# Performance work log

Hardware: AMD Instinct MI355X
Metric: run time of the kernel (lower is better)

The kernel has to match this reference:

```python
import jax, jax.numpy as jnp
import numpy as np

HID, HQ, HKV, D, W = 2880, 64, 8, 64, 128  # hidden, q heads, kv heads, head_dim, sliding window
SCALE = D ** -0.5
NEG = -1e30


def _rope(x, cos, sin):
    # x: [B,S,H,D]; cos/sin: [S, D//2]
    c = cos[None, :, None, :].astype(x.dtype)
    s = sin[None, :, None, :].astype(x.dtype)
    x1, x2 = jnp.split(x, 2, axis=-1)
    return jnp.concatenate([x1 * c - x2 * s, x2 * c + x1 * s], axis=-1)


def setup_inputs() -> dict:
    key = jax.random.key(0)
    ks = jax.random.split(key, 12)
    B, S = 1, 4096
    std = 0.02
    x = jax.random.normal(ks[0], (B, S, HID), jnp.float32)
    # realistic rotary table (cos || sin), half-dim each
    inv_freq = 1.0 / (150000.0 ** (np.arange(0, D, 2, dtype=np.float32) / D))
    ang = np.arange(S, dtype=np.float32)[:, None] * inv_freq[None, :]
    freqs_cis = jnp.asarray(np.concatenate([np.cos(ang), np.sin(ang)], axis=-1), jnp.float32)  # [S, D]
    Wq = jax.random.normal(ks[1], (HID, HQ * D), jnp.float32) * std
    bq = jnp.zeros((HQ * D,), jnp.float32)
    Wk = jax.random.normal(ks[2], (HID, HKV * D), jnp.float32) * std
    bk = jnp.zeros((HKV * D,), jnp.float32)
    Wv = jax.random.normal(ks[3], (HID, HKV * D), jnp.float32) * std
    bv = jnp.zeros((HKV * D,), jnp.float32)
    Wo = jax.random.normal(ks[4], (HQ * D, HID), jnp.float32) * std
    bo = jnp.zeros((HID,), jnp.float32)
    sinks = jax.random.normal(ks[5], (HQ,), jnp.float32) * std
    return {"x": x, "freqs_cis": freqs_cis, "Wq": Wq, "bq": bq, "Wk": Wk, "bk": bk,
            "Wv": Wv, "bv": bv, "Wo": Wo, "bo": bo, "sinks": sinks}


def reference(x, freqs_cis, Wq, bq, Wk, bk, Wv, bv, Wo, bo, sinks):
    B, S, _ = x.shape
    G = HQ // HKV
    nb = S // W  # S must be a multiple of W
    cos, sin = jnp.split(freqs_cis, 2, axis=-1)

    q = (x @ Wq + bq).reshape(B, S, HQ, D)
    k = (x @ Wk + bk).reshape(B, S, HKV, D)
    v = (x @ Wv + bv).reshape(B, S, HKV, D)
    q = _rope(q, cos, sin)
    k = _rope(k, cos, sin)

    q = q.transpose(0, 2, 1, 3)  # [B,HQ,S,D]
    k = k.transpose(0, 2, 1, 3)  # [B,HKV,S,D]
    v = v.transpose(0, 2, 1, 3)

    # blocked sliding-window: each query block of size W sees keys [blk*W - W, blk*W + W)
    qb = q.reshape(B, HKV, G, nb, W, D)
    kp = jnp.pad(k, ((0, 0), (0, 0), (W, 0), (0, 0)))  # prepend W zero keys
    vp = jnp.pad(v, ((0, 0), (0, 0), (W, 0), (0, 0)))
    widx = jnp.arange(nb)[:, None] * W + jnp.arange(2 * W)[None, :]  # [nb, 2W]
    kb = kp[:, :, widx]  # [B,HKV,nb,2W,D]
    vb = vp[:, :, widx]

    scores = jnp.einsum('bkgntd,bkncd->bkgntc', qb, kb) * SCALE  # [B,HKV,G,nb,W,2W]

    t = jnp.arange(W)[:, None]
    j = jnp.arange(2 * W)[None, :]
    band = (j >= t + 1) & (j <= t + W)  # 0 <= qpos - kpos <= W-1
    kpos_ok = (jnp.arange(nb)[:, None] * W - W + jnp.arange(2 * W)[None, :]) >= 0  # [nb,2W]
    mask = band[None, :, :] & kpos_ok[:, None, :]  # [nb,W,2W]
    scores = jnp.where(mask[None, None, None], scores, NEG)

    sink = sinks.reshape(HKV, G)[None, :, :, None, None]  # [1,HKV,G,1,1]
    m = jnp.maximum(scores.max(axis=-1), sink)  # [B,HKV,G,nb,W]
    e = jnp.exp(scores - m[..., None])
    denom = e.sum(axis=-1) + jnp.exp(sink - m)
    p = e / denom[..., None]

    o = jnp.einsum('bkgntc,bkncd->bkgntd', p, vb)  # [B,HKV,G,nb,W,D]
    o = o.reshape(B, HQ, S, D).transpose(0, 2, 1, 3).reshape(B, S, HQ * D)
    return o @ Wo + bo
```

## Files before the change

### kernel.cpp

```cpp
#include <hip/hip_runtime.h>
#include <hip/hip_bf16.h>
#include <stdint.h>


typedef __attribute__((ext_vector_type(8))) short bf16x8;
typedef __attribute__((ext_vector_type(4))) float f32x4;
typedef __attribute__((ext_vector_type(8))) unsigned short ushort8;

#define DEVI static __device__ __forceinline__

DEVI unsigned short f2bf(float f) {
  unsigned x = __float_as_uint(f);
  return (unsigned short)((x + 0x7fffu + ((x >> 16) & 1u)) >> 16);
}
DEVI float bf2f(unsigned short u) { return __uint_as_float(((unsigned)u) << 16); }

DEVI void async16(const void* g, void* l) {
  __builtin_amdgcn_global_load_lds(
      (const __attribute__((address_space(1))) void*)g,
      (__attribute__((address_space(3))) void*)l, 16, 0, 0);
}

__global__ void k_cast_bf16(const float* __restrict__ src,
                            unsigned short* __restrict__ dst, long n) {
  long i = ((long)blockIdx.x * blockDim.x + threadIdx.x) * 4;
  const long stride = (long)gridDim.x * blockDim.x * 4;
  for (; i < n; i += stride) {
    float4 v = *(const float4*)(src + i);
    ushort4 o = make_ushort4(f2bf(v.x), f2bf(v.y), f2bf(v.z), f2bf(v.w));
    *(ushort4*)(dst + i) = o;
  }
}

__global__ void k_transpose_cast(const float* __restrict__ src,
                                 unsigned short* __restrict__ dst,
                                 int R, int C) {
  __shared__ float tile[64][65];
  const int t = threadIdx.x;
  const int r0 = blockIdx.y * 64, c0 = blockIdx.x * 64;
#pragma unroll
  for (int i = 0; i < 16; i++) {
    int r = i * 4 + (t >> 6), c = t & 63;
    float v = 0.f;
    if (c0 + c < C) v = src[(long)(r0 + r) * C + c0 + c];
    tile[r][c] = v;
  }
  __syncthreads();
#pragma unroll
  for (int i = 0; i < 16; i++) {
    int nn = i * 4 + (t >> 6), kk = t & 63;
    dst[(long)(c0 + nn) * R + r0 + kk] = f2bf(tile[kk][nn]);
  }
}

__global__ void k_concat_bias(const float* __restrict__ bq,
                              const float* __restrict__ bk,
                              const float* __restrict__ bv,
                              float* __restrict__ dst) {
  int i = blockIdx.x * 256 + threadIdx.x;
  if (i < 5120)
    dst[i] = (i < 4096) ? bq[i] : ((i < 4608) ? bk[i - 4096] : bv[i - 4608]);
}

#define STG(c, half, t)                                                        \
  do {                                                                         \
    const int tt_ = ((t) < NT) ? (t) : NT - 1;                                 \
    const long ko_ = (long)tt_ * 64;                                           \
    if ((half) < 2) {                                                          \
      const unsigned short* s_ = gA + (long)(half) * 128 * Kd + ko_;           \
      unsigned short* d_ = &As_[c][(((half) * 128) + w8) * 64];                \
      async16(s_, d_);                                                         \
      async16(s_ + 64 * (long)Kd, d_ + 64 * 64);                               \
    } else {                                                                   \
      const unsigned short* s_ = gB + (long)((half) - 2) * 128 * Kd + ko_;     \
      unsigned short* d_ = &Bs_[c][((((half) - 2) * 128) + w8) * 64];          \
      async16(s_, d_);                                                         \
      async16(s_ + 64 * (long)Kd, d_ + 64 * 64);                               \
    }                                                                          \
  } while (0)

#define LOADA(c, mh)                                                           \
  do {                                                                         \
    _Pragma("unroll") for (int m4 = 0; m4 < 4; m4++) {                         \
      const unsigned short* r_ =                                               \
          &As_[c][(wr128 + ((mh)*4 + m4) * 16 + ll) * 64];                     \
      aF[m4][0] = *(const bf16x8*)(r_ + sl0 * 8);                              \
      aF[m4][1] = *(const bf16x8*)(r_ + sl1 * 8);                              \
    }                                                                          \
  } while (0)

#define LOADB(c, nh)                                                           \
  do {                                                                         \
    _Pragma("unroll") for (int n2 = 0; n2 < 2; n2++) {                         \
      const unsigned short* r_ =                                               \
          &Bs_[c][(wc64 + ((nh)*2 + n2) * 16 + ll) * 64];                      \
      bF[nh][n2][0] = *(const bf16x8*)(r_ + sl0 * 8);                          \
      bF[nh][n2][1] = *(const bf16x8*)(r_ + sl1 * 8);                          \
    }                                                                          \
  } while (0)

#define MFMAQ(mh, nh)                                                          \
  do {                                                                         \
    __builtin_amdgcn_s_setprio(1);                                             \
    _Pragma("unroll") for (int m4 = 0; m4 < 4; m4++)                           \
        _Pragma("unroll") for (int n2 = 0; n2 < 2; n2++) {                     \
      acc[(mh)*4 + m4][(nh)*2 + n2] = __builtin_amdgcn_mfma_f32_16x16x32_bf16( \
          aF[m4][0], bF[nh][n2][0], acc[(mh)*4 + m4][(nh)*2 + n2], 0, 0, 0);   \
      acc[(mh)*4 + m4][(nh)*2 + n2] = __builtin_amdgcn_mfma_f32_16x16x32_bf16( \
          aF[m4][1], bF[nh][n2][1], acc[(mh)*4 + m4][(nh)*2 + n2], 0, 0, 0);   \
    }                                                                          \
    __builtin_amdgcn_s_setprio(0);                                             \
  } while (0)

#define BAR() __builtin_amdgcn_s_barrier()
#define VMW4() asm volatile("s_waitcnt vmcnt(4)" ::: "memory")

template <bool OUT_BF16, bool NMASK>
__global__ __launch_bounds__(512, 2) void k_gemm8(
    const unsigned short* __restrict__ A, const unsigned short* __restrict__ Bt,
    const float* __restrict__ bias, void* __restrict__ Cout,
    int Kd, int TMX, int TNX, int ldc, int Nreal) {
  __shared__ unsigned short As_[2][256 * 64];
  __shared__ unsigned short Bs_[2][256 * 64];
  const int tid = threadIdx.x;
  const int w = tid >> 6, l = tid & 63;
  const int wr = w >> 2, wc = w & 3;
  const int lg = l >> 4, ll = l & 15;
  const int w8 = w * 8;
  const int wr128 = wr * 128, wc64 = wc * 64;
  const int sl0 = lg ^ (ll & 7), sl1 = sl0 ^ 4;
  const int NT = Kd >> 6;

  const int b = blockIdx.x;
  const int x = b & 7, r = b >> 3;
  const int tm = (x >> 1) * TMX + (r % TMX);
  const int tn = (x & 1) * TNX + (r / TMX);
  const long m0 = (long)tm * 256, n0 = (long)tn * 256;

  const unsigned short* gA =
      A + (m0 + (tid >> 3)) * (long)Kd + (((tid & 7) ^ ((tid >> 3) & 7)) << 3);
  const unsigned short* gB =
      Bt + (n0 + (tid >> 3)) * (long)Kd + (((tid & 7) ^ ((tid >> 3) & 7)) << 3);

  f32x4 acc[8][4];
#pragma unroll
  for (int i = 0; i < 8; i++)
#pragma unroll
    for (int j = 0; j < 4; j++) acc[i][j] = (f32x4){0.f, 0.f, 0.f, 0.f};
  bf16x8 aF[4][2], bF[2][2][2];

  STG(0, 0, 0); STG(0, 1, 0); STG(0, 2, 0); STG(0, 3, 0);
  STG(1, 2, 1); STG(1, 3, 1);
  VMW4();
  BAR();

  const int NITER = NT >> 1;
  for (int i = 0; i < NITER; i++) {
    const int t = 2 * i;
    LOADA(0, 0); LOADB(0, 0); STG(1, 0, t + 1); BAR(); MFMAQ(0, 0); BAR();
    LOADB(0, 1);              STG(1, 1, t + 1); BAR(); MFMAQ(0, 1); BAR();
    LOADA(0, 1);              STG(0, 2, t + 2); BAR(); MFMAQ(1, 1); BAR();
                              STG(0, 3, t + 2); BAR(); MFMAQ(1, 0); VMW4(); BAR();
    LOADA(1, 0); LOADB(1, 0); STG(0, 0, t + 2); BAR(); MFMAQ(0, 0); BAR();
    LOADB(1, 1);              STG(0, 1, t + 2); BAR(); MFMAQ(0, 1); BAR();
    LOADA(1, 1);              STG(1, 2, t + 3); BAR(); MFMAQ(1, 1); BAR();
                              STG(1, 3, t + 3); BAR(); MFMAQ(1, 0); VMW4(); BAR();
  }
  if (NT & 1) {
    LOADA(0, 0); LOADB(0, 0); MFMAQ(0, 0);
    LOADB(0, 1); MFMAQ(0, 1);
    LOADA(0, 1); MFMAQ(1, 1);
    MFMAQ(1, 0);
  }

#pragma unroll
  for (int nn = 0; nn < 4; nn++) {
    int col = (int)n0 + wc64 + nn * 16 + ll;
    bool ok = (!NMASK) || (col < Nreal);
    float bv_ = ok ? bias[col] : 0.f;
#pragma unroll
    for (int m = 0; m < 8; m++) {
      long row = m0 + wr128 + m * 16 + lg * 4;
#pragma unroll
      for (int j = 0; j < 4; j++) {
        float v = acc[m][nn][j] + bv_;
        if (ok) {
          if (OUT_BF16)
            ((unsigned short*)Cout)[(row + j) * (long)ldc + col] = f2bf(v);
          else
            ((float*)Cout)[(row + j) * (long)ldc + col] = v;
        }
      }
    }
  }
}

__global__ void k_rope(unsigned short* __restrict__ qkv,
                       const float* __restrict__ fc) {
  const int s = blockIdx.x;
  const float* f = fc + (long)s * 64;
  unsigned short* row = qkv + (long)s * 5120;
  const int i = threadIdx.x;
  if (i < 288) {
    const int hh = i >> 2, g = (i & 3) * 8;
    ushort8 a = *(const ushort8*)&row[hh * 64 + g];
    ushort8 b = *(const ushort8*)&row[hh * 64 + 32 + g];
    ushort8 ra, rb;
#pragma unroll
    for (int e = 0; e < 8; e++) {
      float c = f[g + e], sn = f[32 + g + e];
      float x1 = bf2f(a[e]), x2 = bf2f(b[e]);
      ra[e] = f2bf(x1 * c - x2 * sn);
      rb[e] = f2bf(x2 * c + x1 * sn);
    }
    *(ushort8*)&row[hh * 64 + g] = ra;
    *(ushort8*)&row[hh * 64 + 32 + g] = rb;
  }
}

__global__ void k_transpose_v(const unsigned short* __restrict__ qkv,
                              unsigned short* __restrict__ vt) {
  __shared__ unsigned short tile[64][72];
  const int t = threadIdx.x;
  const int ts = blockIdx.x;
  const int tj = blockIdx.y;
#pragma unroll
  for (int i = 0; i < 2; i++) {
    int s = i * 32 + (t >> 3), j = (t & 7) * 8;
    *(ushort8*)&tile[s][j] =
        *(const ushort8*)(qkv + (long)(ts * 64 + s) * 5120 + 4608 + tj * 64 + j);
  }
  __syncthreads();
  int j = t >> 2, s0 = (t & 3) * 16;
  ushort8 v0, v1;
#pragma unroll
  for (int x = 0; x < 8; x++) {
    v0[x] = tile[s0 + x][j];
    v1[x] = tile[s0 + 8 + x][j];
  }
  unsigned short* dst = vt + (long)(tj * 64 + j) * 4096 + ts * 64 + s0;
  *(ushort8*)dst = v0;
  *(ushort8*)(dst + 8) = v1;
}

__global__ __launch_bounds__(256) void k_attn(
    const unsigned short* __restrict__ qkv, const unsigned short* __restrict__ vt,
    const float* __restrict__ sinks, unsigned short* __restrict__ o) {
  __shared__ unsigned short Ps[4][32][136];
  __shared__ unsigned short Ks[128][72];
  __shared__ unsigned short Vts[64][136];
  unsigned short(*Qs)[72] = (unsigned short(*)[72]) & Ps[0][0][0];

  const int n = blockIdx.x, h = blockIdx.y;
  const int kvh = h >> 3;
  const int t = threadIdx.x, w = t >> 6, l = t & 63;
  const int lg = l >> 4, ll = l & 15;
  const int w2 = 2 * w;

#pragma unroll
  for (int i = 0; i < 4; i++) {
    int s = 32 * i + (t >> 3), c8 = (t & 7) * 8;
    *(ushort8*)&Qs[s][c8] =
        *(const ushort8*)(qkv + (long)(n * 128 + s) * 5120 + h * 64 + c8);
  }
  __syncthreads();
  bf16x8 aq[2][2];
#pragma unroll
  for (int m = 0; m < 2; m++)
#pragma unroll
    for (int ks = 0; ks < 2; ks++)
      aq[m][ks] = *(const bf16x8*)&Qs[32 * w + 16 * m + ll][32 * ks + 8 * lg];

  f32x4 oacc[2][4];
#pragma unroll
  for (int m = 0; m < 2; m++)
#pragma unroll
    for (int nt = 0; nt < 4; nt++) oacc[m][nt] = (f32x4){0.f, 0.f, 0.f, 0.f};
  float mrun[2][4], lrun[2][4];
#pragma unroll
  for (int m = 0; m < 2; m++)
#pragma unroll
    for (int j = 0; j < 4; j++) { mrun[m][j] = -3.0e38f; lrun[m][j] = 0.f; }

#pragma unroll
  for (int ch = 0; ch < 2; ch++) {
    if (ch == 0 && n == 0) continue;
    const int kbase = (n - 1 + ch) * 128;
#pragma unroll
    for (int i = 0; i < 4; i++) {
      int c = 32 * i + (t >> 3), c8 = (t & 7) * 8;
      *(ushort8*)&Ks[c][c8] = *(const ushort8*)(
          qkv + (long)(kbase + c) * 5120 + 4096 + kvh * 64 + c8);
    }
#pragma unroll
    for (int i = 0; i < 4; i++) {
      int d = 16 * i + (t >> 4), c8 = (t & 15) * 8;
      *(ushort8*)&Vts[d][c8] =
          *(const ushort8*)(vt + (long)(kvh * 64 + d) * 4096 + kbase + c8);
    }
    __syncthreads();

    f32x4 sacc[2][8];
#pragma unroll
    for (int m = 0; m < 2; m++)
#pragma unroll
      for (int ct = 0; ct < 8; ct++) sacc[m][ct] = (f32x4){0.f, 0.f, 0.f, 0.f};
#pragma unroll
    for (int ct = 0; ct < 8; ct++) {
      const bool pvkeep = (ch == 0) ? (ct >= w2) : (ct <= w2 + 1);
      if (!pvkeep) continue;
      bf16x8 bk0 = *(const bf16x8*)&Ks[16 * ct + ll][8 * lg];
      bf16x8 bk1 = *(const bf16x8*)&Ks[16 * ct + ll][32 + 8 * lg];
#pragma unroll
      for (int m = 0; m < 2; m++) {
        const bool qkv_ok = (ch == 0) ? (ct >= w2 + m) : (ct <= w2 + m);
        if (qkv_ok) {
          sacc[m][ct] = __builtin_amdgcn_mfma_f32_16x16x32_bf16(
              aq[m][0], bk0, sacc[m][ct], 0, 0, 0);
          sacc[m][ct] = __builtin_amdgcn_mfma_f32_16x16x32_bf16(
              aq[m][1], bk1, sacc[m][ct], 0, 0, 0);
        }
      }
    }

    float cmax[2][4];
#pragma unroll
    for (int m = 0; m < 2; m++)
#pragma unroll
      for (int j = 0; j < 4; j++) cmax[m][j] = -3.0e38f;
#pragma unroll
    for (int m = 0; m < 2; m++)
#pragma unroll
      for (int ct = 0; ct < 8; ct++) {
        const bool pvkeep = (ch == 0) ? (ct >= w2) : (ct <= w2 + 1);
        if (!pvkeep) continue;
#pragma unroll
        for (int j = 0; j < 4; j++) {
          int trow = 32 * w + 16 * m + 4 * lg + j;
          int cc = ch * 128 + 16 * ct + ll;
          bool valid = (cc >= trow + 1) && (cc <= trow + 128);
          float sv = valid ? sacc[m][ct][j] * 0.125f : -1.0e30f;
          sacc[m][ct][j] = sv;
          cmax[m][j] = fmaxf(cmax[m][j], sv);
        }
      }
#pragma unroll
    for (int m = 0; m < 2; m++)
#pragma unroll
      for (int j = 0; j < 4; j++) {
        float v = cmax[m][j];
#pragma unroll
        for (int off = 1; off < 16; off <<= 1) v = fmaxf(v, __shfl_xor(v, off));
        cmax[m][j] = v;
      }

    float fsc[2][4];
#pragma unroll
    for (int m = 0; m < 2; m++)
#pragma unroll
      for (int j = 0; j < 4; j++) {
        float mnew = fmaxf(mrun[m][j], cmax[m][j]);
        fsc[m][j] = __expf(mrun[m][j] - mnew);
        mrun[m][j] = mnew;
        lrun[m][j] *= fsc[m][j];
      }

    float psum[2][4];
#pragma unroll
    for (int m = 0; m < 2; m++)
#pragma unroll
      for (int j = 0; j < 4; j++) psum[m][j] = 0.f;
#pragma unroll
    for (int m = 0; m < 2; m++)
#pragma unroll
      for (int ct = 0; ct < 8; ct++) {
        const bool pvkeep = (ch == 0) ? (ct >= w2) : (ct <= w2 + 1);
        if (!pvkeep) continue;
#pragma unroll
        for (int j = 0; j < 4; j++) {
          float p = __expf(sacc[m][ct][j] - mrun[m][j]);
          psum[m][j] += p;
          Ps[w][16 * m + 4 * lg + j][16 * ct + ll] = f2bf(p);
        }
      }
#pragma unroll
    for (int m = 0; m < 2; m++)
#pragma unroll
      for (int j = 0; j < 4; j++) {
        float v = psum[m][j];
#pragma unroll
        for (int off = 1; off < 16; off <<= 1) v += __shfl_xor(v, off);
        lrun[m][j] += v;
#pragma unroll
        for (int nt = 0; nt < 4; nt++) oacc[m][nt][j] *= fsc[m][j];
      }

    asm volatile("s_waitcnt lgkmcnt(0)" ::: "memory");

#pragma unroll
    for (int ks = 0; ks < 4; ks++) {
      const bool keep = (ch == 0) ? (ks >= w) : (ks <= w);
      if (!keep) continue;
      bf16x8 pa[2], vb[4];
#pragma unroll
      for (int m = 0; m < 2; m++)
        pa[m] = *(const bf16x8*)&Ps[w][16 * m + ll][32 * ks + 8 * lg];
#pragma unroll
      for (int nt = 0; nt < 4; nt++)
        vb[nt] = *(const bf16x8*)&Vts[16 * nt + ll][32 * ks + 8 * lg];
#pragma unroll
      for (int m = 0; m < 2; m++)
#pragma unroll
        for (int nt = 0; nt < 4; nt++)
          oacc[m][nt] = __builtin_amdgcn_mfma_f32_16x16x32_bf16(
              pa[m], vb[nt], oacc[m][nt], 0, 0, 0);
    }
    __syncthreads();
  }

  const float sk = sinks[h];
#pragma unroll
  for (int m = 0; m < 2; m++)
#pragma unroll
    for (int j = 0; j < 4; j++) {
      float mf = fmaxf(mrun[m][j], sk);
      float f = __expf(mrun[m][j] - mf);
      float denom = lrun[m][j] * f + __expf(sk - mf);
      float sc = f / denom;
#pragma unroll
      for (int nt = 0; nt < 4; nt++) oacc[m][nt][j] *= sc;
    }
#pragma unroll
  for (int m = 0; m < 2; m++)
#pragma unroll
    for (int nt = 0; nt < 4; nt++)
#pragma unroll
      for (int j = 0; j < 4; j++) {
        long row = (long)n * 128 + 32 * w + 16 * m + 4 * lg + j;
        int col = h * 64 + 16 * nt + ll;
        o[row * 4096 + col] = f2bf(oacc[m][nt][j]);
      }
}

extern "C" void kernel_launch(void* const* d_in, const int* in_sizes, int n_in,
                              void* d_out, int out_size, void* d_ws,
                              size_t ws_size, hipStream_t stream) {
  const float* x = (const float*)d_in[0];
  const float* fc = (const float*)d_in[1];
  const float* Wq = (const float*)d_in[2];
  const float* bq = (const float*)d_in[3];
  const float* Wk = (const float*)d_in[4];
  const float* bk = (const float*)d_in[5];
  const float* Wv = (const float*)d_in[6];
  const float* bv = (const float*)d_in[7];
  const float* Wo = (const float*)d_in[8];
  const float* bo = (const float*)d_in[9];
  const float* sinks = (const float*)d_in[10];
  float* out = (float*)d_out;

  char* p = (char*)d_ws;
  unsigned short* xb = (unsigned short*)p;
  unsigned short* obuf = (unsigned short*)p;
  p += (size_t)4096 * 2880 * 2;
  unsigned short* Wqkvt = (unsigned short*)p;  p += (size_t)5120 * 2880 * 2;
  unsigned short* Wot = (unsigned short*)p;    p += (size_t)3072 * 4096 * 2;
  unsigned short* qkv = (unsigned short*)p;    p += (size_t)4096 * 5120 * 2;
  unsigned short* vt = (unsigned short*)p;     p += (size_t)512 * 4096 * 2;
  float* biasq = (float*)p;                    p += (size_t)5120 * 4;

  k_cast_bf16<<<2048, 256, 0, stream>>>(x, xb, (long)4096 * 2880);
  k_transpose_cast<<<dim3(64, 45), 256, 0, stream>>>(Wq, Wqkvt, 2880, 4096);
  k_transpose_cast<<<dim3(8, 45), 256, 0, stream>>>(
      Wk, Wqkvt + (size_t)4096 * 2880, 2880, 512);
  k_transpose_cast<<<dim3(8, 45), 256, 0, stream>>>(
      Wv, Wqkvt + (size_t)4608 * 2880, 2880, 512);
  k_transpose_cast<<<dim3(48, 64), 256, 0, stream>>>(Wo, Wot, 4096, 2880);
  k_concat_bias<<<20, 256, 0, stream>>>(bq, bk, bv, biasq);

  k_gemm8<true, false><<<320, 512, 0, stream>>>(
      xb, Wqkvt, biasq, qkv, 2880, 4, 10, 5120, 5120);

  k_rope<<<4096, 320, 0, stream>>>(qkv, fc);
  k_transpose_v<<<dim3(64, 8), 256, 0, stream>>>(qkv, vt);

  k_attn<<<dim3(32, 64), 256, 0, stream>>>(qkv, vt, sinks, obuf);

  k_gemm8<false, true><<<192, 512, 0, stream>>>(
      obuf, Wot, bo, out, 4096, 4, 6, 2880, 2880);
}
```

Measured before the change: 586.0 us.

## Use non-square GEMM N-tiles to fit the CU count and drop padding

Makes the GEMM kernel's N-tile width a template parameter (NREP*64 columns) and rewrites the async staging into 64-row slabs with a new interleaved load schedule and wait counts. The QKV projection now uses 256x320 tiles in 256 blocks and the output projection uses 256x192 tiles in 240 blocks, so both grids match the GPU's compute units more closely. Tiles now cover N exactly, which removes the column masking and the padded Wo buffer. The changed staging order and vmcnt values add a risk of pipeline hazards, and the wider B tile raises register and LDS pressure.

```diff
diff --git a/kernel.cpp b/kernel.cpp
--- a/kernel.cpp
+++ b/kernel.cpp
@@ -62,21 +62,24 @@
     dst[i] = (i < 4096) ? bq[i] : ((i < 4608) ? bk[i - 4096] : bv[i - 4608]);
 }
 
-#define STG(c, half, t)                                                        \
+#define SA(c, slab, t)                                                         \
   do {                                                                         \
     const int tt_ = ((t) < NT) ? (t) : NT - 1;                                 \
-    const long ko_ = (long)tt_ * 64;                                           \
-    if ((half) < 2) {                                                          \
-      const unsigned short* s_ = gA + (long)(half) * 128 * Kd + ko_;           \
-      unsigned short* d_ = &As_[c][(((half) * 128) + w8) * 64];                \
-      async16(s_, d_);                                                         \
-      async16(s_ + 64 * (long)Kd, d_ + 64 * 64);                               \
-    } else {                                                                   \
-      const unsigned short* s_ = gB + (long)((half) - 2) * 128 * Kd + ko_;     \
-      unsigned short* d_ = &Bs_[c][((((half) - 2) * 128) + w8) * 64];          \
-      async16(s_, d_);                                                         \
-      async16(s_ + 64 * (long)Kd, d_ + 64 * 64);                               \
-    }                                                                          \
+    async16(gA + (long)(slab)*64 * Kd + (long)tt_ * 64,                        \
+            &As_[c][((slab)*64 + w8) * 64]);                                   \
+  } while (0)
+
+#define SB(c, slab, t)                                                         \
+  do {                                                                         \
+    const int tt_ = ((t) < NT) ? (t) : NT - 1;                                 \
+    async16(gB + (long)(slab)*64 * Kd + (long)tt_ * 64,                        \
+            &Bs_[c][((slab)*64 + w8) * 64]);                                   \
+  } while (0)
+
+#define SBHI(c, t)                                                             \
+  do {                                                                         \
+    SB(c, 2, t);                                                               \
+    if constexpr (NREP > 3) { SB(c, 3, t); SB(c, 4, t); }                      \
   } while (0)
 
 #define LOADA(c, mh)                                                           \
@@ -91,80 +94,109 @@
 
 #define LOADB(c, nh)                                                           \
   do {                                                                         \
-    _Pragma("unroll") for (int n2 = 0; n2 < 2; n2++) {                         \
-      const unsigned short* r_ =                                               \
-          &Bs_[c][(wc64 + ((nh)*2 + n2) * 16 + ll) * 64];                      \
-      bF[nh][n2][0] = *(const bf16x8*)(r_ + sl0 * 8);                          \
-      bF[nh][n2][1] = *(const bf16x8*)(r_ + sl1 * 8);                          \
+    constexpr int F0_ = (nh) ? NQ0 : 0;                                        \
+    constexpr int F1_ = (nh) ? NREP : NQ0;                                     \
+    _Pragma("unroll") for (int f = F0_; f < F1_; f++) {                        \
+      const unsigned short* r_ = &Bs_[c][(wcN + f * 16 + ll) * 64];            \
+      bF[nh][f - F0_][0] = *(const bf16x8*)(r_ + sl0 * 8);                     \
+      bF[nh][f - F0_][1] = *(const bf16x8*)(r_ + sl1 * 8);                     \
     }                                                                          \
   } while (0)
 
 #define MFMAQ(mh, nh)                                                          \
   do {                                                                         \
+    constexpr int F0_ = (nh) ? NQ0 : 0;                                        \
+    constexpr int F1_ = (nh) ? NREP : NQ0;                                     \
     __builtin_amdgcn_s_setprio(1);                                             \
     _Pragma("unroll") for (int m4 = 0; m4 < 4; m4++)                           \
-        _Pragma("unroll") for (int n2 = 0; n2 < 2; n2++) {                     \
-      acc[(mh)*4 + m4][(nh)*2 + n2] = __builtin_amdgcn_mfma_f32_16x16x32_bf16( \
-          aF[m4][0], bF[nh][n2][0], acc[(mh)*4 + m4][(nh)*2 + n2], 0, 0, 0);   \
-      acc[(mh)*4 + m4][(nh)*2 + n2] = __builtin_amdgcn_mfma_f32_16x16x32_bf16( \
-          aF[m4][1], bF[nh][n2][1], acc[(mh)*4 + m4][(nh)*2 + n2], 0, 0, 0);   \
+        _Pragma("unroll") for (int f = F0_; f < F1_; f++) {                    \
+      acc[(mh)*4 + m4][f] = __builtin_amdgcn_mfma_f32_16x16x32_bf16(           \
+          aF[m4][0], bF[nh][f - F0_][0], acc[(mh)*4 + m4][f], 0, 0, 0);        \
+      acc[(mh)*4 + m4][f] = __builtin_amdgcn_mfma_f32_16x16x32_bf16(           \
+          aF[m4][1], bF[nh][f - F0_][1], acc[(mh)*4 + m4][f], 0, 0, 0);        \
     }                                                                          \
     __builtin_amdgcn_s_setprio(0);                                             \
   } while (0)
 
 #define BAR() __builtin_amdgcn_s_barrier()
-#define VMW4() asm volatile("s_waitcnt vmcnt(4)" ::: "memory")
-
-template <bool OUT_BF16, bool NMASK>
+#define VMW()                                                                  \
+  do {                                                                         \
+    if constexpr (NREP == 5)                                                   \
+      asm volatile("s_waitcnt vmcnt(7)" ::: "memory");                         \
+    else                                                                       \
+      asm volatile("s_waitcnt vmcnt(5)" ::: "memory");                         \
+  } while (0)
+
+template <int NREP, int NQ0, bool OUT_BF16, int MAP>
 __global__ __launch_bounds__(512, 2) void k_gemm8(
     const unsigned short* __restrict__ A, const unsigned short* __restrict__ Bt,
     const float* __restrict__ bias, void* __restrict__ Cout,
-    int Kd, int TMX, int TNX, int ldc, int Nreal) {
+    int Kd, int ldc, int NTN) {
+  constexpr int BROWS = NREP * 64;
   __shared__ unsigned short As_[2][256 * 64];
-  __shared__ unsigned short Bs_[2][256 * 64];
+  __shared__ unsigned short Bs_[2][BROWS * 64];
   const int tid = threadIdx.x;
   const int w = tid >> 6, l = tid & 63;
   const int wr = w >> 2, wc = w & 3;
   const int lg = l >> 4, ll = l & 15;
   const int w8 = w * 8;
-  const int wr128 = wr * 128, wc64 = wc * 64;
+  const int wr128 = wr * 128;
+  const int wcN = wc * (NREP * 16);
   const int sl0 = lg ^ (ll & 7), sl1 = sl0 ^ 4;
   const int NT = Kd >> 6;
 
+  int tm, tn;
   const int b = blockIdx.x;
   const int x = b & 7, r = b >> 3;
-  const int tm = (x >> 1) * TMX + (r % TMX);
-  const int tn = (x & 1) * TNX + (r / TMX);
-  const long m0 = (long)tm * 256, n0 = (long)tn * 256;
+  if (MAP == 0) {
+    tm = (x >> 1) * 4 + (r & 3);
+    tn = (x & 1) * 8 + (r >> 2);
+  } else {
+    const int t_ = x * (gridDim.x >> 3) + r;
+    tm = t_ / NTN;
+    tn = t_ % NTN;
+  }
+  const long m0 = (long)tm * 256, n0 = (long)tn * BROWS;
 
   const unsigned short* gA =
       A + (m0 + (tid >> 3)) * (long)Kd + (((tid & 7) ^ ((tid >> 3) & 7)) << 3);
   const unsigned short* gB =
       Bt + (n0 + (tid >> 3)) * (long)Kd + (((tid & 7) ^ ((tid >> 3) & 7)) << 3);
 
-  f32x4 acc[8][4];
+  f32x4 acc[8][NREP];
 #pragma unroll
   for (int i = 0; i < 8; i++)
 #pragma unroll
-    for (int j = 0; j < 4; j++) acc[i][j] = (f32x4){0.f, 0.f, 0.f, 0.f};
-  bf16x8 aF[4][2], bF[2][2][2];
-
-  STG(0, 0, 0); STG(0, 1, 0); STG(0, 2, 0); STG(0, 3, 0);
-  STG(1, 2, 1); STG(1, 3, 1);
-  VMW4();
+    for (int j = 0; j < NREP; j++) acc[i][j] = (f32x4){0.f, 0.f, 0.f, 0.f};
+  bf16x8 aF[4][2], bF[2][NQ0][2];
+
+  SA(0, 0, 0); SA(0, 1, 0); SA(0, 2, 0); SA(0, 3, 0);
+  SB(0, 0, 0); SB(0, 1, 0); SBHI(0, 0);
+  SA(1, 0, 1); SA(1, 2, 1);
+  SB(1, 0, 1); SB(1, 1, 1); SBHI(1, 1);
+  VMW();
   BAR();
 
   const int NITER = NT >> 1;
   for (int i = 0; i < NITER; i++) {
     const int t = 2 * i;
-    LOADA(0, 0); LOADB(0, 0); STG(1, 0, t + 1); BAR(); MFMAQ(0, 0); BAR();
-    LOADB(0, 1);              STG(1, 1, t + 1); BAR(); MFMAQ(0, 1); BAR();
-    LOADA(0, 1);              STG(0, 2, t + 2); BAR(); MFMAQ(1, 1); BAR();
-                              STG(0, 3, t + 2); BAR(); MFMAQ(1, 0); VMW4(); BAR();
-    LOADA(1, 0); LOADB(1, 0); STG(0, 0, t + 2); BAR(); MFMAQ(0, 0); BAR();
-    LOADB(1, 1);              STG(0, 1, t + 2); BAR(); MFMAQ(0, 1); BAR();
-    LOADA(1, 1);              STG(1, 2, t + 3); BAR(); MFMAQ(1, 1); BAR();
-                              STG(1, 3, t + 3); BAR(); MFMAQ(1, 0); VMW4(); BAR();
+    LOADA(0, 0); LOADB(0, 0); SA(1, 1, t + 1); SA(1, 3, t + 1);
+    BAR(); MFMAQ(0, 0); BAR();
+    LOADB(0, 1); SA(0, 0, t + 2); SA(0, 2, t + 2);
+    BAR(); MFMAQ(0, 1); BAR();
+    LOADA(0, 1); SB(0, 0, t + 2); SB(0, 1, t + 2);
+    BAR(); MFMAQ(1, 1); BAR();
+    SBHI(0, t + 2);
+    BAR(); MFMAQ(1, 0); VMW(); BAR();
+
+    LOADA(1, 0); LOADB(1, 0); SA(0, 1, t + 2); SA(0, 3, t + 2);
+    BAR(); MFMAQ(0, 0); BAR();
+    LOADB(1, 1); SA(1, 0, t + 3); SA(1, 2, t + 3);
+    BAR(); MFMAQ(0, 1); BAR();
+    LOADA(1, 1); SB(1, 0, t + 3); SB(1, 1, t + 3);
+    BAR(); MFMAQ(1, 1); BAR();
+    SBHI(1, t + 3);
+    BAR(); MFMAQ(1, 0); VMW(); BAR();
   }
   if (NT & 1) {
     LOADA(0, 0); LOADB(0, 0); MFMAQ(0, 0);
@@ -172,24 +204,22 @@
     LOADA(0, 1); MFMAQ(1, 1);
     MFMAQ(1, 0);
   }
-
-#pragma unroll
-  for (int nn = 0; nn < 4; nn++) {
-    int col = (int)n0 + wc64 + nn * 16 + ll;
-    bool ok = (!NMASK) || (col < Nreal);
-    float bv_ = ok ? bias[col] : 0.f;
+  asm volatile("s_waitcnt vmcnt(0)" ::: "memory");
+
+#pragma unroll
+  for (int nn = 0; nn < NREP; nn++) {
+    int col = (int)n0 + wcN + nn * 16 + ll;
+    float bv_ = bias[col];
 #pragma unroll
     for (int m = 0; m < 8; m++) {
       long row = m0 + wr128 + m * 16 + lg * 4;
 #pragma unroll
       for (int j = 0; j < 4; j++) {
         float v = acc[m][nn][j] + bv_;
-        if (ok) {
-          if (OUT_BF16)
-            ((unsigned short*)Cout)[(row + j) * (long)ldc + col] = f2bf(v);
-          else
-            ((float*)Cout)[(row + j) * (long)ldc + col] = v;
-        }
+        if (OUT_BF16)
+          ((unsigned short*)Cout)[(row + j) * (long)ldc + col] = f2bf(v);
+        else
+          ((float*)Cout)[(row + j) * (long)ldc + col] = v;
       }
     }
   }
@@ -463,7 +493,7 @@
   unsigned short* obuf = (unsigned short*)p;
   p += (size_t)4096 * 2880 * 2;
   unsigned short* Wqkvt = (unsigned short*)p;  p += (size_t)5120 * 2880 * 2;
-  unsigned short* Wot = (unsigned short*)p;    p += (size_t)3072 * 4096 * 2;
+  unsigned short* Wot = (unsigned short*)p;    p += (size_t)2880 * 4096 * 2;
   unsigned short* qkv = (unsigned short*)p;    p += (size_t)4096 * 5120 * 2;
   unsigned short* vt = (unsigned short*)p;     p += (size_t)512 * 4096 * 2;
   float* biasq = (float*)p;                    p += (size_t)5120 * 4;
@@ -474,17 +504,17 @@
       Wk, Wqkvt + (size_t)4096 * 2880, 2880, 512);
   k_transpose_cast<<<dim3(8, 45), 256, 0, stream>>>(
       Wv, Wqkvt + (size_t)4608 * 2880, 2880, 512);
-  k_transpose_cast<<<dim3(48, 64), 256, 0, stream>>>(Wo, Wot, 4096, 2880);
+  k_transpose_cast<<<dim3(45, 64), 256, 0, stream>>>(Wo, Wot, 4096, 2880);
   k_concat_bias<<<20, 256, 0, stream>>>(bq, bk, bv, biasq);
 
-  k_gemm8<true, false><<<320, 512, 0, stream>>>(
-      xb, Wqkvt, biasq, qkv, 2880, 4, 10, 5120, 5120);
+  k_gemm8<5, 3, true, 0><<<256, 512, 0, stream>>>(
+      xb, Wqkvt, biasq, qkv, 2880, 5120, 16);
 
   k_rope<<<4096, 320, 0, stream>>>(qkv, fc);
   k_transpose_v<<<dim3(64, 8), 256, 0, stream>>>(qkv, vt);
 
   k_attn<<<dim3(32, 64), 256, 0, stream>>>(qkv, vt, sinks, obuf);
 
-  k_gemm8<false, true><<<192, 512, 0, stream>>>(
-      obuf, Wot, bo, out, 4096, 4, 6, 2880, 2880);
-}
+  k_gemm8<3, 2, false, 1><<<240, 512, 0, stream>>>(
+      obuf, Wot, bo, out, 4096, 2880, 15);
+}
```

Result: slower. 662.6 us (+13.1%).
